# Kernel tuning notes

Measured on AMD Instinct MI355X. Metric: run time of the kernel, lower is better.

The kernel has to match this reference:

```python
import jax, jax.numpy as jnp
import numpy as np

IGNORE = -100000.0


def setup_inputs() -> dict:
    key = jax.random.key(0)
    ks = jax.random.split(key, 5)
    b, s, d_model = 4, 2048, 2048
    n_q, n_kv, d_head = 32, 8, 64
    std = 0.02
    return {
        "normalized_resid_pre": jax.random.normal(ks[0], (b, s, d_model), jnp.float32),
        "W_Q": jax.random.normal(ks[1], (n_q, d_model, d_head), jnp.float32) * std,
        "W_K": jax.random.normal(ks[2], (n_kv, d_model, d_head), jnp.float32) * std,
        "W_V": jax.random.normal(ks[3], (n_kv, d_model, d_head), jnp.float32) * std,
        "W_O": jax.random.normal(ks[4], (n_kv, d_head, d_model), jnp.float32) * std,
    }


def reference(normalized_resid_pre, W_Q, W_K, W_V, W_O):
    x = normalized_resid_pre
    b, s, _ = x.shape
    n_kv, d_head = W_K.shape[0], W_K.shape[2]
    n_q = W_Q.shape[0]
    g = n_q // n_kv

    q = jnp.einsum("bpd,hdk->bphk", x, W_Q)  # [b,s,n_q,d_head]
    k = jnp.einsum("bpd,ndk->bpnk", x, W_K)  # [b,s,n_kv,d_head]
    v = jnp.einsum("bpd,ndk->bpnk", x, W_V)  # [b,s,n_kv,d_head]

    # rearrange: head axis splits as (n_kv_heads, g_size), then moved to [b,s,g,n_kv,d_head]
    gq = q.reshape(b, s, n_kv, g, d_head).transpose(0, 1, 3, 2, 4)

    # NOTE: faithful to source — g axis is SUMMED in this einsum
    scores = jnp.einsum("bqgnh,bknh->bnqk", gq, k) / jnp.sqrt(jnp.float32(d_head))

    causal = jnp.triu(jnp.ones((s, s), dtype=bool), k=1)  # True above diagonal
    scores = jnp.where(causal, IGNORE, scores)
    pattern = jax.nn.softmax(scores, axis=-1)  # [b,n_kv,q,k]

    z = jnp.einsum("bknh,bnqk->bqnh", v, pattern)  # [b,s,n_kv,d_head]
    attn_out = jnp.einsum("bqnh,nhd->bqd", z, W_O)  # [b,s,d_model]
    return attn_out
```

## Files before the change

### kernel.cpp

```cpp
#include <hip/hip_runtime.h>

typedef __attribute__((ext_vector_type(8))) _Float16 half8;
typedef __attribute__((ext_vector_type(4))) float f32x4;

#define BATCH  4
#define SLEN   2048
#define DMODEL 2048
#define NKV    8
#define GRP    4
#define DH     64
#define QKV    1536
#define KVDIM  512
#define MROWS  (BATCH * SLEN)

__device__ __forceinline__ unsigned short f2h(float f) {
    union { _Float16 h; unsigned short u; } cv;
    cv.h = (_Float16)f;
    return cv.u;
}

__device__ __forceinline__ void gl16(const void* g, void* l) {
    __builtin_amdgcn_global_load_lds(
        (const __attribute__((address_space(1))) void*)g,
        (__attribute__((address_space(3))) void*)l, 16, 0, 0);
}

typedef __attribute__((ext_vector_type(4))) short short4v;
union U64S4 { unsigned long long u; short4v s; };

__global__ __launch_bounds__(256) void k_packT(const float* __restrict__ wq,
                                               const float* __restrict__ wk,
                                               const float* __restrict__ wv,
                                               unsigned short* __restrict__ outT) {
    __shared__ float T[64][65];
    const int d0 = blockIdx.x * 64;
    const int ct = blockIdx.y;
    const int mat = ct >> 3, n = ct & 7;
    const int tr = threadIdx.x >> 6, tc = threadIdx.x & 63;
#pragma unroll
    for (int i = 0; i < 16; ++i) {
        int row = tr + i * 4;
        float v;
        if (mat == 0) {
            v = 0.0f;
#pragma unroll
            for (int g = 0; g < GRP; ++g)
                v += wq[((size_t)(n * GRP + g) * DMODEL + d0 + row) * DH + tc];
        } else if (mat == 1) {
            v = wk[((size_t)n * DMODEL + d0 + row) * DH + tc];
        } else {
            v = wv[((size_t)n * DMODEL + d0 + row) * DH + tc];
        }
        T[row][tc] = v;
    }
    __syncthreads();
    const int rr = tc;
#pragma unroll
    for (int i = 0; i < 16; ++i) {
        int cc = tr + i * 4;
        outT[(size_t)(mat * 512 + n * 64 + cc) * DMODEL + d0 + rr] = f2h(T[rr][cc]);
    }
}

__global__ __launch_bounds__(256) void k_transconv_h(const float* __restrict__ in,
                                                     unsigned short* __restrict__ outT,
                                                     int R, int C) {
    __shared__ float T[64][65];
    const int r0 = blockIdx.x * 64, c0 = blockIdx.y * 64;
    const int tr = threadIdx.x >> 6, tc = threadIdx.x & 63;
#pragma unroll
    for (int i = 0; i < 16; ++i)
        T[tr + i * 4][tc] = in[(size_t)(r0 + tr + i * 4) * C + c0 + tc];
    __syncthreads();
    const int rr = tc;
#pragma unroll
    for (int i = 0; i < 16; ++i) {
        int cc = tr + i * 4;
        outT[(size_t)(c0 + cc) * R + r0 + rr] = f2h(T[rr][cc]);
    }
}

__global__ __launch_bounds__(256) void k_convh(const float* __restrict__ in,
                                               unsigned short* __restrict__ out,
                                               int n4) {
    int i = blockIdx.x * 256 + threadIdx.x;
    if (i >= n4) return;
    float4 v = ((const float4*)in)[i];
    ushort4 o;
    o.x = f2h(v.x); o.y = f2h(v.y); o.z = f2h(v.z); o.w = f2h(v.w);
    ((ushort4*)out)[i] = o;
}

__device__ __forceinline__ void stage_rows(const unsigned short* __restrict__ src,
                                           unsigned short* lds, int t, int K,
                                           int k0, int nslots4) {
#pragma unroll
    for (int j = 0; j < 8; ++j) {
        if (j >= nslots4) break;
        int slot = j * 256 + t;
        int row = slot >> 3, blk = slot & 7;
        int c = blk ^ (row & 7);
        gl16(src + (size_t)row * K + k0 + c * 8, lds + slot * 8);
    }
}

__global__ __launch_bounds__(256) void k_gemm_qkv(
        const unsigned short* __restrict__ Ag, const unsigned short* __restrict__ Bg,
        unsigned short* __restrict__ qk, unsigned short* __restrict__ vT) {
    __shared__ unsigned short A2[2][128 * 64];
    __shared__ unsigned short B2[2][192 * 64];

    const int t = threadIdx.x;
    const size_t m0 = (size_t)blockIdx.x * 128, n0 = (size_t)blockIdx.y * 192;
    const int w = t >> 6, l = t & 63;
    const int wm = (w >> 1) * 64, wn = (w & 1) * 96;
    const int r = l & 15, q = l >> 4;
    f32x4 acc[4][6] = {};
    const int K = DMODEL;
    const int NT = K / 64;

    stage_rows(Ag + m0 * K, A2[0], t, K, 0, 4);
    stage_rows(Bg + n0 * K, B2[0], t, K, 0, 6);
    asm volatile("s_waitcnt vmcnt(0)" ::: "memory");
    __builtin_amdgcn_s_barrier();
    int cur = 0;
    for (int kt = 0; kt < NT; ++kt) {
        if (kt + 1 < NT) {
            stage_rows(Ag + m0 * K, A2[cur ^ 1], t, K, (kt + 1) * 64, 4);
            stage_rows(Bg + n0 * K, B2[cur ^ 1], t, K, (kt + 1) * 64, 6);
        }
        const unsigned short* Ac = A2[cur];
        const unsigned short* Bc = B2[cur];
        half8 af[4][2], bf[6][2];
#pragma unroll
        for (int i = 0; i < 4; ++i)
#pragma unroll
            for (int ks = 0; ks < 2; ++ks) {
                int ra = wm + i * 16 + r;
                af[i][ks] = *(const half8*)&Ac[ra * 64 + ((((ks << 2) | q) ^ (ra & 7)) << 3)];
            }
#pragma unroll
        for (int j = 0; j < 6; ++j)
#pragma unroll
            for (int ks = 0; ks < 2; ++ks) {
                int rb = wn + j * 16 + r;
                bf[j][ks] = *(const half8*)&Bc[rb * 64 + ((((ks << 2) | q) ^ (rb & 7)) << 3)];
            }
        __builtin_amdgcn_s_setprio(1);
#pragma unroll
        for (int i = 0; i < 4; ++i)
#pragma unroll
            for (int j = 0; j < 6; ++j) {
                acc[i][j] = __builtin_amdgcn_mfma_f32_16x16x32_f16(af[i][0], bf[j][0], acc[i][j], 0, 0, 0);
                acc[i][j] = __builtin_amdgcn_mfma_f32_16x16x32_f16(af[i][1], bf[j][1], acc[i][j], 0, 0, 0);
            }
        __builtin_amdgcn_s_setprio(0);
        asm volatile("s_waitcnt vmcnt(0)" ::: "memory");
        __builtin_amdgcn_s_barrier();
        cur ^= 1;
    }

#pragma unroll
    for (int i = 0; i < 4; ++i)
#pragma unroll
        for (int j = 0; j < 6; ++j) {
            int col = (int)n0 + wn + j * 16 + r;
            size_t rowb = m0 + wm + i * 16 + q * 4;
            if (col < 1024) {
#pragma unroll
                for (int e = 0; e < 4; ++e)
                    qk[(rowb + e) * 1024 + col] = f2h(acc[i][j][e]);
            } else {
                int d = col - 1024;
                ushort4 pk;
                pk.x = f2h(acc[i][j][0]); pk.y = f2h(acc[i][j][1]);
                pk.z = f2h(acc[i][j][2]); pk.w = f2h(acc[i][j][3]);
                *(ushort4*)&vT[(size_t)d * MROWS + rowb] = pk;
            }
        }
}

__global__ __launch_bounds__(256) void k_gemm_out(
        const unsigned short* __restrict__ Ag, const unsigned short* __restrict__ Bg,
        float* __restrict__ C) {
    __shared__ unsigned short A2[2][128 * 64];
    __shared__ unsigned short B2[2][128 * 64];

    const int t = threadIdx.x;
    const size_t m0 = (size_t)blockIdx.x * 128, n0 = (size_t)blockIdx.y * 128;
    const int w = t >> 6, l = t & 63;
    const int wm = (w >> 1) * 64, wn = (w & 1) * 64;
    const int r = l & 15, q = l >> 4;
    f32x4 acc[4][4] = {};
    const int K = KVDIM;
    const int NT = K / 64;

    stage_rows(Ag + m0 * K, A2[0], t, K, 0, 4);
    stage_rows(Bg + n0 * K, B2[0], t, K, 0, 4);
    asm volatile("s_waitcnt vmcnt(0)" ::: "memory");
    __builtin_amdgcn_s_barrier();
    int cur = 0;
    for (int kt = 0; kt < NT; ++kt) {
        if (kt + 1 < NT) {
            stage_rows(Ag + m0 * K, A2[cur ^ 1], t, K, (kt + 1) * 64, 4);
            stage_rows(Bg + n0 * K, B2[cur ^ 1], t, K, (kt + 1) * 64, 4);
        }
        const unsigned short* Ac = A2[cur];
        const unsigned short* Bc = B2[cur];
        half8 af[4][2], bf[4][2];
#pragma unroll
        for (int i = 0; i < 4; ++i)
#pragma unroll
            for (int ks = 0; ks < 2; ++ks) {
                int ra = wm + i * 16 + r;
                af[i][ks] = *(const half8*)&Ac[ra * 64 + ((((ks << 2) | q) ^ (ra & 7)) << 3)];
                int rb = wn + i * 16 + r;
                bf[i][ks] = *(const half8*)&Bc[rb * 64 + ((((ks << 2) | q) ^ (rb & 7)) << 3)];
            }
        __builtin_amdgcn_s_setprio(1);
#pragma unroll
        for (int i = 0; i < 4; ++i)
#pragma unroll
            for (int j = 0; j < 4; ++j) {
                acc[i][j] = __builtin_amdgcn_mfma_f32_16x16x32_f16(af[i][0], bf[j][0], acc[i][j], 0, 0, 0);
                acc[i][j] = __builtin_amdgcn_mfma_f32_16x16x32_f16(af[i][1], bf[j][1], acc[i][j], 0, 0, 0);
            }
        __builtin_amdgcn_s_setprio(0);
        asm volatile("s_waitcnt vmcnt(0)" ::: "memory");
        __builtin_amdgcn_s_barrier();
        cur ^= 1;
    }

#pragma unroll
    for (int i = 0; i < 4; ++i)
#pragma unroll
        for (int j = 0; j < 4; ++j) {
            int col = (int)n0 + wn + j * 16 + r;
            size_t rowb = m0 + wm + i * 16 + q * 4;
#pragma unroll
            for (int e = 0; e < 4; ++e)
                C[(rowb + e) * DMODEL + col] = acc[i][j][e];
        }
}

__global__ __launch_bounds__(256) void k_attn_mfma(
        const unsigned short* __restrict__ qk, const unsigned short* __restrict__ vT,
        unsigned short* __restrict__ zh) {
    __shared__ unsigned short Ks[2][128 * 64];
    __shared__ unsigned short Vs[2][64 * 128];
    __shared__ unsigned short Pt[4 * 128 * 16];

    const int t  = threadIdx.x;
    const int w  = t >> 6, l = t & 63;
    const int p  = blockIdx.x;
    const int n  = blockIdx.y, b = blockIdx.z;
    const int r  = l & 15, g = l >> 4;
    const int wq0 = w * 16;

#define STAGE_KV(buf, kr0)                                                    \
    _Pragma("unroll") for (int j2 = 0; j2 < 4; ++j2) {                        \
        int s2 = j2 * 256 + t;                                                \
        int rK = s2 >> 3, cK = (s2 & 7) ^ (rK & 7);                           \
        gl16(qk + ((kr0) + rK) * 1024 + 512 + n * 64 + cK * 8,                \
             &Ks[buf][s2 * 8]);                                               \
        int rV = s2 >> 4, cV = (s2 & 15) ^ (rV & 15);                         \
        gl16(vT + (size_t)(n * 64 + rV) * MROWS + (kr0) + cV * 8,             \
             &Vs[buf][s2 * 8]);                                               \
    }

#pragma unroll 1
    for (int seg = 0; seg < 2; ++seg) {
        const int qt = seg ? p : (31 - p);
        const int nkt = (qt + 2) >> 1;
        const size_t qrow0 = (size_t)(b * SLEN + qt * 64);

        half8 qh[2];
#pragma unroll
        for (int ks = 0; ks < 2; ++ks) {
            size_t off = (qrow0 + wq0 + r) * 1024 + n * 64 + ks * 32 + g * 8;
            qh[ks] = *(const half8*)(qk + off);
#pragma unroll
            for (int e2 = 0; e2 < 8; ++e2) qh[ks][e2] = qh[ks][e2] * (_Float16)0.125f;
        }

        STAGE_KV(0, (size_t)(b * SLEN))
        asm volatile("s_waitcnt vmcnt(0)" ::: "memory");
        __builtin_amdgcn_s_barrier();

        float m_[4], lsum[4];
#pragma unroll
        for (int e = 0; e < 4; ++e) { m_[e] = -3.0e38f; lsum[e] = 0.0f; }
        f32x4 accz[4] = {};

        for (int kt = 0; kt < nkt; ++kt) {
            const int cur = kt & 1;
            if (kt + 1 < nkt) {
                STAGE_KV(cur ^ 1, (size_t)(b * SLEN + (kt + 1) * 128))
            }
            const unsigned short* Ksc = Ks[cur];
            const unsigned short* Vsc = Vs[cur];

            f32x4 s[8] = {};
#pragma unroll
            for (int ct = 0; ct < 8; ++ct)
#pragma unroll
                for (int ks = 0; ks < 2; ++ks) {
                    int row = ct * 16 + r;
                    int off = row * 128 + (((ks * 4 + g) ^ (row & 7)) << 4);
                    half8 kh8 = *(const half8*)((char*)Ksc + off);
                    s[ct] = __builtin_amdgcn_mfma_f32_16x16x32_f16(qh[ks], kh8, s[ct], 0, 0, 0);
                }

            if (kt == nkt - 1) {
#pragma unroll
                for (int ct = 0; ct < 8; ++ct)
#pragma unroll
                    for (int e = 0; e < 4; ++e)
                        if ((kt * 128 + ct * 16 + r) > (qt * 64 + wq0 + g * 4 + e))
                            s[ct][e] = -100000.0f;
            }

            float al[4], nm[4];
#pragma unroll
            for (int e = 0; e < 4; ++e) {
                float pm = fmaxf(fmaxf(fmaxf(s[0][e], s[1][e]), fmaxf(s[2][e], s[3][e])),
                                 fmaxf(fmaxf(s[4][e], s[5][e]), fmaxf(s[6][e], s[7][e])));
                pm = fmaxf(pm, __shfl_xor(pm, 1));
                pm = fmaxf(pm, __shfl_xor(pm, 2));
                pm = fmaxf(pm, __shfl_xor(pm, 4));
                pm = fmaxf(pm, __shfl_xor(pm, 8));
                nm[e] = fmaxf(m_[e], pm);
                al[e] = __expf(m_[e] - nm[e]);
                m_[e] = nm[e];
            }
            {
                int src = (r >> 2) << 4;
                float a0 = __shfl(al[0], src), a1 = __shfl(al[1], src);
                float a2 = __shfl(al[2], src), a3 = __shfl(al[3], src);
                float ax = (r & 1) ? a1 : a0, ay = (r & 1) ? a3 : a2;
                float aq = (r & 2) ? ay : ax;
#pragma unroll
                for (int dt = 0; dt < 4; ++dt) {
                    accz[dt][0] *= aq; accz[dt][1] *= aq;
                    accz[dt][2] *= aq; accz[dt][3] *= aq;
                }
            }

            float ps[4] = {};
#pragma unroll
            for (int ct = 0; ct < 8; ++ct) {
                float p0 = __expf(s[ct][0] - m_[0]);
                float p1 = __expf(s[ct][1] - m_[1]);
                float p2 = __expf(s[ct][2] - m_[2]);
                float p3 = __expf(s[ct][3] - m_[3]);
                ps[0] += p0; ps[1] += p1; ps[2] += p2; ps[3] += p3;
                short4v pk = { (short)f2h(p0), (short)f2h(p1),
                               (short)f2h(p2), (short)f2h(p3) };
                int kv = ct * 16 + r;
                int phys = (kv >> 5) * 32 + (((kv >> 2) & 1) << 4)
                         + (((kv >> 3) & 3) << 2) + (kv & 3);
                *(short4v*)((char*)Pt + w * 4096 + phys * 32 + g * 8) = pk;
            }

#pragma unroll
            for (int e = 0; e < 4; ++e) {
                float rs = ps[e];
                rs += __shfl_xor(rs, 1); rs += __shfl_xor(rs, 2);
                rs += __shfl_xor(rs, 4); rs += __shfl_xor(rs, 8);
                lsum[e] = lsum[e] * al[e] + rs;
            }

            asm volatile("s_waitcnt lgkmcnt(0)" ::: "memory");
            __builtin_amdgcn_sched_barrier(0);
#pragma unroll
            for (int ks = 0; ks < 4; ++ks) {
                unsigned base = (unsigned)(size_t)((char*)Pt + w * 4096 + ks * 1024) + l * 8;
                U64S4 t1, t2;
                asm volatile("ds_read_b64_tr_b16 %0, %1" : "=v"(t1.u) : "v"(base) : "memory");
                asm volatile("ds_read_b64_tr_b16 %0, %1" : "=v"(t2.u) : "v"(base + 512) : "memory");
                asm volatile("s_waitcnt lgkmcnt(0)" ::: "memory");
                __builtin_amdgcn_sched_barrier(0);
                short4v pa = t1.s, pb = t2.s;
                union { short s[8]; half8 h; } pf;
                pf.s[0] = pa[0]; pf.s[1] = pa[1]; pf.s[2] = pa[2]; pf.s[3] = pa[3];
                pf.s[4] = pb[0]; pf.s[5] = pb[1]; pf.s[6] = pb[2]; pf.s[7] = pb[3];
#pragma unroll
                for (int dt = 0; dt < 4; ++dt) {
                    int d = dt * 16 + r;
                    int off = d * 256 + (((ks * 4 + g) ^ (d & 15)) << 4);
                    half8 vfrag = *(const half8*)((char*)Vsc + off);
                    accz[dt] = __builtin_amdgcn_mfma_f32_16x16x32_f16(vfrag, pf.h, accz[dt], 0, 0, 0);
                }
            }

            asm volatile("s_waitcnt vmcnt(0)" ::: "memory");
            __builtin_amdgcn_s_barrier();
        }

        int src = (r >> 2) << 4;
        float l0 = __shfl(lsum[0], src), l1 = __shfl(lsum[1], src);
        float l2 = __shfl(lsum[2], src), l3 = __shfl(lsum[3], src);
        float lx = (r & 1) ? l1 : l0, ly = (r & 1) ? l3 : l2;
        float inv = 1.0f / ((r & 2) ? ly : lx);
#pragma unroll
        for (int dt = 0; dt < 4; ++dt) {
            ushort4 h4;
#pragma unroll
            for (int e = 0; e < 4; ++e)
                ((unsigned short*)&h4)[e] = f2h(accz[dt][e] * inv);
            size_t off = (qrow0 + wq0 + r) * 512 + n * 64 + dt * 16 + g * 4;
            *(ushort4*)(zh + off) = h4;
        }
    }
#undef STAGE_KV
}

extern "C" void kernel_launch(void* const* d_in, const int* in_sizes, int n_in,
                              void* d_out, int out_size, void* d_ws, size_t ws_size,
                              hipStream_t stream) {
    const float* x  = (const float*)d_in[0];
    const float* wq = (const float*)d_in[1];
    const float* wk = (const float*)d_in[2];
    const float* wv = (const float*)d_in[3];
    const float* wo = (const float*)d_in[4];
    float* out = (float*)d_out;

    char* w = (char*)d_ws;
    unsigned short* xh  = (unsigned short*)(w);
    unsigned short* zh  = (unsigned short*)(w);
    unsigned short* qk  = (unsigned short*)(w + 33554432);
    unsigned short* vT  = (unsigned short*)(w + 50331648);
    unsigned short* wcatT = (unsigned short*)(w + 58720256);
    unsigned short* woT = (unsigned short*)(w + 65011712);

    k_packT<<<dim3(32, 24), 256, 0, stream>>>(wq, wk, wv, wcatT);
    k_transconv_h<<<dim3(8, 32), 256, 0, stream>>>(wo, woT, KVDIM, DMODEL);
    k_convh<<<dim3(16384), 256, 0, stream>>>(x, xh, MROWS * DMODEL / 4);
    k_gemm_qkv<<<dim3(64, 8), 256, 0, stream>>>(xh, wcatT, qk, vT);
    k_attn_mfma<<<dim3(16, NKV, BATCH), 256, 0, stream>>>(qk, vT, zh);
    k_gemm_out<<<dim3(64, 16), 256, 0, stream>>>(zh, woT, out);
}
```

Before: 187.8 us.

## Use 32x32x16 MFMA with 2-wave blocks and BK=32 in QKV GEMM

Rewrites the QKV projection GEMM to run two waves per block, each computing a 128x96 tile with 32x32x16 MFMAs instead of four waves using 16x16x32 MFMAs, and halves the K-tile to 32 with a matching LDS swizzle. The larger MFMA shape raises arithmetic per LDS fragment load and the smaller LDS footprint is meant to allow two blocks per CU. The cost is more accumulator registers per wave, twice as many K-loop iterations and barriers, and fewer waves per block to hide latency.

```diff
diff --git a/kernel.cpp b/kernel.cpp
--- a/kernel.cpp
+++ b/kernel.cpp
@@ -2,6 +2,7 @@
 
 typedef __attribute__((ext_vector_type(8))) _Float16 half8;
 typedef __attribute__((ext_vector_type(4))) float f32x4;
+typedef __attribute__((ext_vector_type(16))) float f32x16;
 
 #define BATCH  4
 #define SLEN   2048
@@ -104,57 +105,68 @@
     }
 }
 
-__global__ __launch_bounds__(256) void k_gemm_qkv(
+__device__ __forceinline__ void stage_rows32(const unsigned short* __restrict__ src,
+                                             unsigned short* lds, int t, int K,
+                                             int k0, int niter) {
+#pragma unroll
+    for (int j = 0; j < 8; ++j) {
+        if (j >= niter) break;
+        int slot = j * 128 + t;
+        int row = slot >> 2, blk = slot & 3;
+        int c = blk ^ (row & 3);
+        gl16(src + (size_t)row * K + k0 + c * 8, lds + slot * 8);
+    }
+}
+
+__global__ __launch_bounds__(128, 2) void k_gemm_qkv(
         const unsigned short* __restrict__ Ag, const unsigned short* __restrict__ Bg,
         unsigned short* __restrict__ qk, unsigned short* __restrict__ vT) {
-    __shared__ unsigned short A2[2][128 * 64];
-    __shared__ unsigned short B2[2][192 * 64];
+    __shared__ unsigned short A2[2][128 * 32];
+    __shared__ unsigned short B2[2][192 * 32];
 
     const int t = threadIdx.x;
     const size_t m0 = (size_t)blockIdx.x * 128, n0 = (size_t)blockIdx.y * 192;
     const int w = t >> 6, l = t & 63;
-    const int wm = (w >> 1) * 64, wn = (w & 1) * 96;
-    const int r = l & 15, q = l >> 4;
-    f32x4 acc[4][6] = {};
+    const int wn = w * 96;
+    const int r2 = l & 31, q2 = l >> 5;
+    f32x16 acc[4][3] = {};
     const int K = DMODEL;
-    const int NT = K / 64;
-
-    stage_rows(Ag + m0 * K, A2[0], t, K, 0, 4);
-    stage_rows(Bg + n0 * K, B2[0], t, K, 0, 6);
+    const int NT = K / 32;
+
+    stage_rows32(Ag + m0 * K, A2[0], t, K, 0, 4);
+    stage_rows32(Bg + n0 * K, B2[0], t, K, 0, 6);
     asm volatile("s_waitcnt vmcnt(0)" ::: "memory");
     __builtin_amdgcn_s_barrier();
     int cur = 0;
     for (int kt = 0; kt < NT; ++kt) {
         if (kt + 1 < NT) {
-            stage_rows(Ag + m0 * K, A2[cur ^ 1], t, K, (kt + 1) * 64, 4);
-            stage_rows(Bg + n0 * K, B2[cur ^ 1], t, K, (kt + 1) * 64, 6);
+            stage_rows32(Ag + m0 * K, A2[cur ^ 1], t, K, (kt + 1) * 32, 4);
+            stage_rows32(Bg + n0 * K, B2[cur ^ 1], t, K, (kt + 1) * 32, 6);
         }
         const unsigned short* Ac = A2[cur];
         const unsigned short* Bc = B2[cur];
-        half8 af[4][2], bf[6][2];
-#pragma unroll
-        for (int i = 0; i < 4; ++i)
-#pragma unroll
-            for (int ks = 0; ks < 2; ++ks) {
-                int ra = wm + i * 16 + r;
-                af[i][ks] = *(const half8*)&Ac[ra * 64 + ((((ks << 2) | q) ^ (ra & 7)) << 3)];
-            }
-#pragma unroll
-        for (int j = 0; j < 6; ++j)
-#pragma unroll
-            for (int ks = 0; ks < 2; ++ks) {
-                int rb = wn + j * 16 + r;
-                bf[j][ks] = *(const half8*)&Bc[rb * 64 + ((((ks << 2) | q) ^ (rb & 7)) << 3)];
-            }
-        __builtin_amdgcn_s_setprio(1);
-#pragma unroll
-        for (int i = 0; i < 4; ++i)
-#pragma unroll
-            for (int j = 0; j < 6; ++j) {
-                acc[i][j] = __builtin_amdgcn_mfma_f32_16x16x32_f16(af[i][0], bf[j][0], acc[i][j], 0, 0, 0);
-                acc[i][j] = __builtin_amdgcn_mfma_f32_16x16x32_f16(af[i][1], bf[j][1], acc[i][j], 0, 0, 0);
-            }
-        __builtin_amdgcn_s_setprio(0);
+#pragma unroll
+        for (int ks = 0; ks < 2; ++ks) {
+            half8 af[4], bf[3];
+#pragma unroll
+            for (int i = 0; i < 4; ++i) {
+                int ra = i * 32 + r2;
+                af[i] = *(const half8*)&Ac[ra * 32 + (((ks * 2 + q2) ^ (ra & 3)) << 3)];
+            }
+#pragma unroll
+            for (int j = 0; j < 3; ++j) {
+                int rb = wn + j * 32 + r2;
+                bf[j] = *(const half8*)&Bc[rb * 32 + (((ks * 2 + q2) ^ (rb & 3)) << 3)];
+            }
+            __builtin_amdgcn_s_setprio(1);
+#pragma unroll
+            for (int i = 0; i < 4; ++i)
+#pragma unroll
+                for (int j = 0; j < 3; ++j)
+                    acc[i][j] = __builtin_amdgcn_mfma_f32_32x32x16_f16(
+                        af[i], bf[j], acc[i][j], 0, 0, 0);
+            __builtin_amdgcn_s_setprio(0);
+        }
         asm volatile("s_waitcnt vmcnt(0)" ::: "memory");
         __builtin_amdgcn_s_barrier();
         cur ^= 1;
@@ -163,19 +175,26 @@
 #pragma unroll
     for (int i = 0; i < 4; ++i)
 #pragma unroll
-        for (int j = 0; j < 6; ++j) {
-            int col = (int)n0 + wn + j * 16 + r;
-            size_t rowb = m0 + wm + i * 16 + q * 4;
+        for (int j = 0; j < 3; ++j) {
+            int col = (int)n0 + wn + j * 32 + (l & 31);
+            size_t rowb = m0 + i * 32 + q2 * 4;
             if (col < 1024) {
 #pragma unroll
-                for (int e = 0; e < 4; ++e)
-                    qk[(rowb + e) * 1024 + col] = f2h(acc[i][j][e]);
+                for (int e = 0; e < 16; ++e) {
+                    int rr = (e & 3) + 8 * (e >> 2);
+                    qk[(rowb + rr) * 1024 + col] = f2h(acc[i][j][e]);
+                }
             } else {
                 int d = col - 1024;
-                ushort4 pk;
-                pk.x = f2h(acc[i][j][0]); pk.y = f2h(acc[i][j][1]);
-                pk.z = f2h(acc[i][j][2]); pk.w = f2h(acc[i][j][3]);
-                *(ushort4*)&vT[(size_t)d * MROWS + rowb] = pk;
+#pragma unroll
+                for (int e4 = 0; e4 < 4; ++e4) {
+                    ushort4 pk;
+                    pk.x = f2h(acc[i][j][e4 * 4 + 0]);
+                    pk.y = f2h(acc[i][j][e4 * 4 + 1]);
+                    pk.z = f2h(acc[i][j][e4 * 4 + 2]);
+                    pk.w = f2h(acc[i][j][e4 * 4 + 3]);
+                    *(ushort4*)&vT[(size_t)d * MROWS + rowb + 8 * e4] = pk;
+                }
             }
         }
 }
@@ -436,7 +455,7 @@
     k_packT<<<dim3(32, 24), 256, 0, stream>>>(wq, wk, wv, wcatT);
     k_transconv_h<<<dim3(8, 32), 256, 0, stream>>>(wo, woT, KVDIM, DMODEL);
     k_convh<<<dim3(16384), 256, 0, stream>>>(x, xh, MROWS * DMODEL / 4);
-    k_gemm_qkv<<<dim3(64, 8), 256, 0, stream>>>(xh, wcatT, qk, vT);
+    k_gemm_qkv<<<dim3(64, 8), 128, 0, stream>>>(xh, wcatT, qk, vT);
     k_attn_mfma<<<dim3(16, NKV, BATCH), 256, 0, stream>>>(qk, vT, zh);
     k_gemm_out<<<dim3(64, 16), 256, 0, stream>>>(zh, woT, out);
 }
```

After: 212.2 us. +13.0%, slower.
